# Kernel tuning notes

Hardware: AMD Instinct MI355X
Metric: run time of the kernel (lower is better)

Reference implementation:

```python
import jax, jax.numpy as jnp
import numpy as np

B, T, D, U = 16, 4096, 256, 256
ZR = 0.1  # zoneout_rate; inference: h_t = h_cand + ZR*(h_prev - h_cand)


def setup_inputs() -> dict:
    key = jax.random.key(0)
    ks = jax.random.split(key, 16)
    def rn(k, shape, s):
        return (jax.random.normal(k, shape, jnp.float32) * s).astype(jnp.float32)
    inp = {"x": jax.random.normal(ks[0], (B, T, D), jnp.float32)}
    dims = [D, U, U]
    i = 1
    for l in range(3):
        inp[f"W{l}"] = rn(ks[i], (dims[l], 3 * U), 0.05); i += 1
        inp[f"U{l}"] = rn(ks[i], (U, 3 * U), 0.05); i += 1
        inp[f"b{l}"] = rn(ks[i], (2, 3 * U), 0.02); i += 1
        inp[f"h0_{l}"] = rn(ks[i], (1, U), 1.0); i += 1  # learnable_state: N(0,1)
    inp["Wd"] = rn(ks[i], (U, D), 0.05); i += 1
    inp["bd"] = rn(ks[i], (D,), 0.02)
    return inp


def _gru_zoneout_layer(x, W, Uk, b, h0):
    """x: [B,T,in]; Keras GRU reset_after=True, gate order (z,r,h).
    Returns sequence of h_cand (cell outputs); carried state is zoneouted."""
    b_in, b_rec = b[0], b[1]
    xg = jnp.einsum('bti,ig->btg', x, W) + b_in  # [B,T,3U] precomputed input gates
    h_init = jnp.broadcast_to(h0, (x.shape[0], h0.shape[-1]))

    def step(h, xg_t):
        rg = h @ Uk + b_rec                       # [B,3U]
        xz, xr, xh = jnp.split(xg_t, 3, axis=-1)
        rz, rr, rh = jnp.split(rg, 3, axis=-1)
        z = jax.nn.sigmoid(xz + rz)
        r = jax.nn.sigmoid(xr + rr)
        hh = jnp.tanh(xh + r * rh)
        h_cand = z * h + (1.0 - z) * hh           # cell output
        h_new = h_cand + ZR * (h - h_cand)        # zoneout (inference)
        return h_new, h_cand

    _, ys = jax.lax.scan(step, h_init, jnp.swapaxes(xg, 0, 1))  # [T,B,U]
    return jnp.swapaxes(ys, 0, 1)


def reference(x, W0, U0, b0, h0_0, W1, U1, b1, h0_1, W2, U2, b2, h0_2, Wd, bd):
    y = _gru_zoneout_layer(x, W0, U0, b0, h0_0)
    y = y + _gru_zoneout_layer(y, W1, U1, b1, h0_1)   # residual, factor 1.0
    y = y + _gru_zoneout_layer(y, W2, U2, b2, h0_2)
    return jnp.einsum('btu,ud->btd', y, Wd) + bd      # linear dense head
```

## Files before the change

kernel.cpp:

```cpp
#include <hip/hip_runtime.h>
#include <cstdint>
#include <cstddef>

#define ZONEOUT 0.1f

typedef __attribute__((ext_vector_type(8))) short bf16x8;
typedef __attribute__((ext_vector_type(4))) float f32x4;
typedef __attribute__((ext_vector_type(4))) unsigned short u16x4;
typedef __attribute__((ext_vector_type(8))) unsigned short u16x8;
typedef __attribute__((ext_vector_type(4))) float float4_;

static constexpr int BB = 16;
static constexpr int TT = 4096;
static constexpr int DD = 256;
static constexpr int UU = 256;
static constexpr int GG = 768;
static constexpr int STR = 280;

__device__ __forceinline__ unsigned short f2bf(float f) {
  unsigned int u = __builtin_bit_cast(unsigned int, f);
  u = u + 0x7fffu + ((u >> 16) & 1u);
  return (unsigned short)(u >> 16);
}
__device__ __forceinline__ float bf2f(unsigned short s) {
  unsigned int u = ((unsigned int)s) << 16;
  return __builtin_bit_cast(float, u);
}
__device__ __forceinline__ float sigm(float x) {
  float e = __builtin_amdgcn_exp2f(-1.4426950408889634f * x);
  return __builtin_amdgcn_rcpf(1.0f + e);
}
__device__ __forceinline__ float tanh_(float x) {
  float e = __builtin_amdgcn_exp2f(2.8853900817779268f * x);
  return 1.0f - 2.0f * __builtin_amdgcn_rcpf(1.0f + e);
}

__device__ __forceinline__ void wg_barrier_lds() {
  asm volatile("s_waitcnt lgkmcnt(0)\n\ts_barrier" ::: "memory");
}

__global__ void transpose_cast_kernel(const float* __restrict__ src,
                                      unsigned short* __restrict__ dst,
                                      int K, int N) {
  int idx = blockIdx.x * blockDim.x + threadIdx.x;
  int total = K * N;
  if (idx < total) {
    int k = idx / N, n = idx - k * N;
    dst[(size_t)n * K + k] = f2bf(src[idx]);
  }
}

__launch_bounds__(256, 2)
__global__ void gates_gemm_kernel(const float* __restrict__ In,
                                  const unsigned short* __restrict__ Wt,
                                  const float* __restrict__ bin,
                                  unsigned short* __restrict__ xgp) {
  __shared__ unsigned short Asm[64 * STR];
  __shared__ unsigned short Bsm[64 * STR];
  const int m0 = blockIdx.x * 64;
  const int n0 = blockIdx.y * 64;
  const int tid = threadIdx.x;
  {
    int row = tid >> 2, cb = (tid & 3) * 64;
    const float* src = In + (size_t)(m0 + row) * DD + cb;
#pragma unroll
    for (int i = 0; i < 16; ++i) {
      float4_ v = *(const float4_*)(src + i * 4);
      u16x4 o;
      o.x = f2bf(v.x); o.y = f2bf(v.y); o.z = f2bf(v.z); o.w = f2bf(v.w);
      *(u16x4*)(&Asm[row * STR + cb + i * 4]) = o;
    }
  }
  {
#pragma unroll
    for (int i = 0; i < 8; ++i) {
      int c = i * 256 + tid;
      int row = c >> 5, part = c & 31;
      u16x8 v = *(const u16x8*)(Wt + (size_t)(n0 + row) * 256 + part * 8);
      *(u16x8*)(&Bsm[row * STR + part * 8]) = v;
    }
  }
  __syncthreads();
  const int w = tid >> 6, l = tid & 63, lr = l & 15, lg = l >> 4;
  f32x4 acc[4] = {};
#pragma unroll
  for (int k0 = 0; k0 < 8; ++k0) {
    bf16x8 a = *(const bf16x8*)(&Asm[(16 * w + lr) * STR + 32 * k0 + 8 * lg]);
#pragma unroll
    for (int ti = 0; ti < 4; ++ti) {
      bf16x8 b = *(const bf16x8*)(&Bsm[(16 * ti + lr) * STR + 32 * k0 + 8 * lg]);
      acc[ti] = __builtin_amdgcn_mfma_f32_16x16x32_bf16(a, b, acc[ti], 0, 0, 0);
    }
  }
#pragma unroll
  for (int ti = 0; ti < 4; ++ti) {
    int gcol = n0 + 16 * ti + lr;
    float bias = bin[gcol];
    int u = gcol & 255, slot = gcol >> 8;
#pragma unroll
    for (int r = 0; r < 4; ++r) {
      int m = m0 + 16 * w + 4 * lg + r;
      xgp[(size_t)m * 1024 + u * 4 + slot] = f2bf(acc[ti][r] + bias);
    }
  }
}

__launch_bounds__(256, 2)
__global__ void head_gemm_kernel(float* __restrict__ y,
                                 const unsigned short* __restrict__ Wdt,
                                 const float* __restrict__ bd) {
  __shared__ unsigned short Asm[64 * STR];
  const int m0 = blockIdx.x * 64;
  const int tid = threadIdx.x;
  {
    int row = tid >> 2, cb = (tid & 3) * 64;
    const float* src = y + (size_t)(m0 + row) * UU + cb;
#pragma unroll
    for (int i = 0; i < 16; ++i) {
      float4_ v = *(const float4_*)(src + i * 4);
      u16x4 o;
      o.x = f2bf(v.x); o.y = f2bf(v.y); o.z = f2bf(v.z); o.w = f2bf(v.w);
      *(u16x4*)(&Asm[row * STR + cb + i * 4]) = o;
    }
  }
  __syncthreads();
  const int w = tid >> 6, l = tid & 63, lr = l & 15, lg = l >> 4;
  f32x4 acc[16] = {};
#pragma unroll
  for (int k0 = 0; k0 < 8; ++k0) {
    bf16x8 a = *(const bf16x8*)(&Asm[(16 * w + lr) * STR + 32 * k0 + 8 * lg]);
#pragma unroll
    for (int ti = 0; ti < 16; ++ti) {
      bf16x8 b = *(const bf16x8*)(Wdt + (size_t)(16 * ti + lr) * 256 + 32 * k0 + 8 * lg);
      acc[ti] = __builtin_amdgcn_mfma_f32_16x16x32_bf16(a, b, acc[ti], 0, 0, 0);
    }
  }
#pragma unroll
  for (int ti = 0; ti < 16; ++ti) {
    int n = 16 * ti + lr;
    float bias = bd[n];
#pragma unroll
    for (int r = 0; r < 4; ++r) {
      int m = m0 + 16 * w + 4 * lg + r;
      y[(size_t)m * DD + n] = acc[ti][r] + bias;
    }
  }
}

__global__ void __attribute__((amdgpu_flat_work_group_size(512, 512), amdgpu_num_vgpr(256)))
gru_scan_kernel(const unsigned short* __restrict__ xgp,
                const unsigned short* __restrict__ Ut,
                const float* __restrict__ brec,
                const float* __restrict__ h0,
                float* __restrict__ y,
                int resid) {
  __shared__ unsigned short Utail[GG * 72];
  __shared__ unsigned short Hsm[2][BB * STR];

  const int tid = threadIdx.x;
  const int w = tid >> 6;
  const int l = tid & 63;
  const int lr = l & 15;
  const int lg = l >> 4;

  for (int i = 0; i < 12; ++i) {
    int c = i * 512 + tid;
    int row = c >> 3, part = c & 7;
    u16x8 v = *(const u16x8*)(Ut + (size_t)row * 256 + 192 + part * 8);
    *(u16x8*)(&Utail[row * 72 + part * 8]) = v;
  }

  f32x4 ufr[2][3][6];
  float bias[2][3];
#pragma unroll
  for (int tri = 0; tri < 2; ++tri) {
    int u = 32 * w + 16 * tri + lr;
#pragma unroll
    for (int g = 0; g < 3; ++g) {
      int n = g * 256 + u;
      bias[tri][g] = brec[n];
#pragma unroll
      for (int k0 = 0; k0 < 6; ++k0)
        ufr[tri][g][k0] = *(const f32x4*)(Ut + (size_t)n * 256 + 32 * k0 + 8 * lg);
    }
  }
#pragma unroll
  for (int tri = 0; tri < 2; ++tri)
#pragma unroll
    for (int g = 0; g < 3; ++g)
#pragma unroll
      for (int k0 = 0; k0 < 6; ++k0)
        asm volatile("" : "+v"(ufr[tri][g][k0]));

  float hprev[2][4];
#pragma unroll
  for (int tri = 0; tri < 2; ++tri) {
    int u = 32 * w + 16 * tri + lr;
    float hv = h0[u];
#pragma unroll
    for (int r = 0; r < 4; ++r) {
      hprev[tri][r] = hv;
      int b = 4 * lg + r;
      Hsm[0][b * STR + u] = f2bf(hv);
    }
  }

  u16x4 xv[2][4];
#pragma unroll
  for (int tri = 0; tri < 2; ++tri) {
    int u = 32 * w + 16 * tri + lr;
#pragma unroll
    for (int r = 0; r < 4; ++r) {
      int b = 4 * lg + r;
      xv[tri][r] = *(const u16x4*)(xgp + ((size_t)b * TT) * 1024 + u * 4);
    }
  }
  wg_barrier_lds();

  for (int t = 0; t < TT; ++t) {
    const unsigned short* cur = &Hsm[t & 1][0];
    unsigned short* nxt = &Hsm[(t + 1) & 1][0];

    float ypref[2][4];
    if (resid) {
#pragma unroll
      for (int tri = 0; tri < 2; ++tri) {
        int u = 32 * w + 16 * tri + lr;
#pragma unroll
        for (int r = 0; r < 4; ++r) {
          int b = 4 * lg + r;
          ypref[tri][r] = y[((size_t)b * TT + t) * UU + u];
        }
      }
    }

    f32x4 acc[2][3];
#pragma unroll
    for (int tri = 0; tri < 2; ++tri)
#pragma unroll
      for (int g = 0; g < 3; ++g) {
        float bv = bias[tri][g];
        acc[tri][g] = (f32x4){bv, bv, bv, bv};
      }
#pragma unroll
    for (int k0 = 0; k0 < 8; ++k0) {
      bf16x8 a = *(const bf16x8*)(&cur[lr * STR + 32 * k0 + 8 * lg]);
      if (k0 < 6) {
#pragma unroll
        for (int tri = 0; tri < 2; ++tri)
#pragma unroll
          for (int g = 0; g < 3; ++g)
            acc[tri][g] = __builtin_amdgcn_mfma_f32_16x16x32_bf16(
                a, __builtin_bit_cast(bf16x8, ufr[tri][g][k0]), acc[tri][g], 0, 0, 0);
      } else {
#pragma unroll
        for (int tri = 0; tri < 2; ++tri)
#pragma unroll
          for (int g = 0; g < 3; ++g) {
            int n = g * 256 + 32 * w + 16 * tri + lr;
            bf16x8 bfr = *(const bf16x8*)(&Utail[n * 72 + (k0 - 6) * 32 + 8 * lg]);
            acc[tri][g] = __builtin_amdgcn_mfma_f32_16x16x32_bf16(a, bfr, acc[tri][g], 0, 0, 0);
          }
      }
    }

    const int tn = (t + 1 < TT) ? t + 1 : t;
#pragma unroll
    for (int tri = 0; tri < 2; ++tri) {
      int u = 32 * w + 16 * tri + lr;
#pragma unroll
      for (int r = 0; r < 4; ++r) {
        int b = 4 * lg + r;
        u16x4 xvv = xv[tri][r];
        xv[tri][r] = *(const u16x4*)(xgp + ((size_t)b * TT + tn) * 1024 + u * 4);
        float xz = bf2f(xvv.x), xr = bf2f(xvv.y), xh = bf2f(xvv.z);
        float h = hprev[tri][r];
        float z = sigm(xz + acc[tri][0][r]);
        float rg = sigm(xr + acc[tri][1][r]);
        float hh = tanh_(xh + rg * acc[tri][2][r]);
        float cand = hh + z * (h - hh);
        float hnew = cand + ZONEOUT * (h - cand);
        hprev[tri][r] = hnew;
        nxt[b * STR + u] = f2bf(hnew);
        float ov = cand;
        if (resid) ov += ypref[tri][r];
        y[((size_t)b * TT + t) * UU + u] = ov;
      }
    }
    wg_barrier_lds();
  }
}

extern "C" void kernel_launch(void* const* d_in, const int* in_sizes, int n_in,
                              void* d_out, int out_size, void* d_ws, size_t ws_size,
                              hipStream_t stream) {
  const float* x = (const float*)d_in[0];
  const float* W[3]  = {(const float*)d_in[1], (const float*)d_in[5], (const float*)d_in[9]};
  const float* Um[3] = {(const float*)d_in[2], (const float*)d_in[6], (const float*)d_in[10]};
  const float* bm[3] = {(const float*)d_in[3], (const float*)d_in[7], (const float*)d_in[11]};
  const float* h0m[3] = {(const float*)d_in[4], (const float*)d_in[8], (const float*)d_in[12]};
  const float* Wd = (const float*)d_in[13];
  const float* bd = (const float*)d_in[14];
  float* out = (float*)d_out;

  char* ws = (char*)d_ws;
  unsigned short* xgp = (unsigned short*)ws;
  size_t off = (size_t)65536 * 1024 * 2;
  unsigned short* Ut[3];
  unsigned short* Wt[3];
  for (int l = 0; l < 3; ++l) { Ut[l] = (unsigned short*)(ws + off); off += (size_t)768 * 256 * 2; }
  for (int l = 0; l < 3; ++l) { Wt[l] = (unsigned short*)(ws + off); off += (size_t)768 * 256 * 2; }
  unsigned short* Wdt = (unsigned short*)(ws + off); off += (size_t)256 * 256 * 2;

  const int tgrid = (768 * 256 + 255) / 256;
  for (int l = 0; l < 3; ++l) {
    hipLaunchKernelGGL(transpose_cast_kernel, dim3(tgrid), dim3(256), 0, stream, Um[l], Ut[l], 256, 768);
    hipLaunchKernelGGL(transpose_cast_kernel, dim3(tgrid), dim3(256), 0, stream, W[l], Wt[l], 256, 768);
  }
  hipLaunchKernelGGL(transpose_cast_kernel, dim3((256 * 256 + 255) / 256), dim3(256), 0, stream,
                     Wd, Wdt, 256, 256);

  for (int l = 0; l < 3; ++l) {
    const float* in_l = (l == 0) ? x : out;
    hipLaunchKernelGGL(gates_gemm_kernel, dim3(1024, 12), dim3(256), 0, stream,
                       in_l, Wt[l], bm[l], xgp);
    hipLaunchKernelGGL(gru_scan_kernel, dim3(1), dim3(512), 0, stream,
                       xgp, Ut[l], bm[l] + 768, h0m[l], out, l ? 1 : 0);
  }
  hipLaunchKernelGGL(head_gemm_kernel, dim3(1024), dim3(256), 0, stream, out, Wdt, bd);
}
```

Measured before the change: 28.20 ms.

## Split GRU scan across 16 waves with one 16-unit tile each

The single-workgroup recurrent scan grows from 8 waves of 512 threads to 16 waves of 1024 threads. Each wave now owns one 16-unit column tile instead of two, which halves per-wave MFMA work and register-resident U fragments on the serial critical path. LDS strides for the hidden state and the U tail also change (280 to 282, 72 to 70) to alter the bank mapping. The cost is a barrier across twice as many waves every timestep and a lower per-thread register budget, since the explicit 256-VGPR attribute is dropped.

```diff
diff --git a/kernel.cpp b/kernel.cpp
--- a/kernel.cpp
+++ b/kernel.cpp
@@ -15,7 +15,8 @@
 static constexpr int DD = 256;
 static constexpr int UU = 256;
 static constexpr int GG = 768;
-static constexpr int STR = 280;
+static constexpr int STR = 282;
+static constexpr int UTS = 70;
 
 __device__ __forceinline__ unsigned short f2bf(float f) {
   unsigned int u = __builtin_bit_cast(unsigned int, f);
@@ -147,14 +148,14 @@
   }
 }
 
-__global__ void __attribute__((amdgpu_flat_work_group_size(512, 512), amdgpu_num_vgpr(256)))
+__global__ void __attribute__((amdgpu_flat_work_group_size(1024, 1024)))
 gru_scan_kernel(const unsigned short* __restrict__ xgp,
                 const unsigned short* __restrict__ Ut,
                 const float* __restrict__ brec,
                 const float* __restrict__ h0,
                 float* __restrict__ y,
                 int resid) {
-  __shared__ unsigned short Utail[GG * 72];
+  __shared__ unsigned short Utail[GG * UTS];
   __shared__ unsigned short Hsm[2][BB * STR];
 
   const int tid = threadIdx.x;
@@ -162,58 +163,48 @@
   const int l = tid & 63;
   const int lr = l & 15;
   const int lg = l >> 4;
-
-  for (int i = 0; i < 12; ++i) {
-    int c = i * 512 + tid;
+  const int u = 16 * w + lr;
+
+#pragma unroll
+  for (int i = 0; i < 6; ++i) {
+    int c = i * 1024 + tid;
     int row = c >> 3, part = c & 7;
     u16x8 v = *(const u16x8*)(Ut + (size_t)row * 256 + 192 + part * 8);
-    *(u16x8*)(&Utail[row * 72 + part * 8]) = v;
-  }
-
-  f32x4 ufr[2][3][6];
-  float bias[2][3];
-#pragma unroll
-  for (int tri = 0; tri < 2; ++tri) {
-    int u = 32 * w + 16 * tri + lr;
-#pragma unroll
-    for (int g = 0; g < 3; ++g) {
-      int n = g * 256 + u;
-      bias[tri][g] = brec[n];
-#pragma unroll
-      for (int k0 = 0; k0 < 6; ++k0)
-        ufr[tri][g][k0] = *(const f32x4*)(Ut + (size_t)n * 256 + 32 * k0 + 8 * lg);
-    }
-  }
-#pragma unroll
-  for (int tri = 0; tri < 2; ++tri)
-#pragma unroll
-    for (int g = 0; g < 3; ++g)
-#pragma unroll
-      for (int k0 = 0; k0 < 6; ++k0)
-        asm volatile("" : "+v"(ufr[tri][g][k0]));
-
-  float hprev[2][4];
-#pragma unroll
-  for (int tri = 0; tri < 2; ++tri) {
-    int u = 32 * w + 16 * tri + lr;
+    *(u16x8*)(&Utail[row * UTS + part * 8]) = v;
+  }
+
+  f32x4 ufr[3][6];
+  float bias[3];
+#pragma unroll
+  for (int g = 0; g < 3; ++g) {
+    int n = g * 256 + u;
+    bias[g] = brec[n];
+#pragma unroll
+    for (int k0 = 0; k0 < 6; ++k0)
+      ufr[g][k0] = *(const f32x4*)(Ut + (size_t)n * 256 + 32 * k0 + 8 * lg);
+  }
+#pragma unroll
+  for (int g = 0; g < 3; ++g)
+#pragma unroll
+    for (int k0 = 0; k0 < 6; ++k0)
+      asm volatile("" : "+v"(ufr[g][k0]));
+
+  float hprev[4];
+  {
     float hv = h0[u];
 #pragma unroll
     for (int r = 0; r < 4; ++r) {
-      hprev[tri][r] = hv;
+      hprev[r] = hv;
       int b = 4 * lg + r;
       Hsm[0][b * STR + u] = f2bf(hv);
     }
   }
 
-  u16x4 xv[2][4];
-#pragma unroll
-  for (int tri = 0; tri < 2; ++tri) {
-    int u = 32 * w + 16 * tri + lr;
-#pragma unroll
-    for (int r = 0; r < 4; ++r) {
-      int b = 4 * lg + r;
-      xv[tri][r] = *(const u16x4*)(xgp + ((size_t)b * TT) * 1024 + u * 4);
-    }
+  u16x4 xv[4];
+#pragma unroll
+  for (int r = 0; r < 4; ++r) {
+    int b = 4 * lg + r;
+    xv[r] = *(const u16x4*)(xgp + ((size_t)b * TT) * 1024 + u * 4);
   }
   wg_barrier_lds();
 
@@ -221,71 +212,57 @@
     const unsigned short* cur = &Hsm[t & 1][0];
     unsigned short* nxt = &Hsm[(t + 1) & 1][0];
 
-    float ypref[2][4];
+    float ypref[4];
     if (resid) {
 #pragma unroll
-      for (int tri = 0; tri < 2; ++tri) {
-        int u = 32 * w + 16 * tri + lr;
-#pragma unroll
-        for (int r = 0; r < 4; ++r) {
-          int b = 4 * lg + r;
-          ypref[tri][r] = y[((size_t)b * TT + t) * UU + u];
-        }
+      for (int r = 0; r < 4; ++r) {
+        int b = 4 * lg + r;
+        ypref[r] = y[((size_t)b * TT + t) * UU + u];
       }
     }
 
-    f32x4 acc[2][3];
-#pragma unroll
-    for (int tri = 0; tri < 2; ++tri)
-#pragma unroll
-      for (int g = 0; g < 3; ++g) {
-        float bv = bias[tri][g];
-        acc[tri][g] = (f32x4){bv, bv, bv, bv};
-      }
+    f32x4 acc[3];
+#pragma unroll
+    for (int g = 0; g < 3; ++g) {
+      float bv = bias[g];
+      acc[g] = (f32x4){bv, bv, bv, bv};
+    }
 #pragma unroll
     for (int k0 = 0; k0 < 8; ++k0) {
       bf16x8 a = *(const bf16x8*)(&cur[lr * STR + 32 * k0 + 8 * lg]);
       if (k0 < 6) {
 #pragma unroll
-        for (int tri = 0; tri < 2; ++tri)
-#pragma unroll
-          for (int g = 0; g < 3; ++g)
-            acc[tri][g] = __builtin_amdgcn_mfma_f32_16x16x32_bf16(
-                a, __builtin_bit_cast(bf16x8, ufr[tri][g][k0]), acc[tri][g], 0, 0, 0);
+        for (int g = 0; g < 3; ++g)
+          acc[g] = __builtin_amdgcn_mfma_f32_16x16x32_bf16(
+              a, __builtin_bit_cast(bf16x8, ufr[g][k0]), acc[g], 0, 0, 0);
       } else {
 #pragma unroll
-        for (int tri = 0; tri < 2; ++tri)
-#pragma unroll
-          for (int g = 0; g < 3; ++g) {
-            int n = g * 256 + 32 * w + 16 * tri + lr;
-            bf16x8 bfr = *(const bf16x8*)(&Utail[n * 72 + (k0 - 6) * 32 + 8 * lg]);
-            acc[tri][g] = __builtin_amdgcn_mfma_f32_16x16x32_bf16(a, bfr, acc[tri][g], 0, 0, 0);
-          }
+        for (int g = 0; g < 3; ++g) {
+          int n = g * 256 + u;
+          bf16x8 bfr = *(const bf16x8*)(&Utail[n * UTS + (k0 - 6) * 32 + 8 * lg]);
+          acc[g] = __builtin_amdgcn_mfma_f32_16x16x32_bf16(a, bfr, acc[g], 0, 0, 0);
+        }
       }
     }
 
     const int tn = (t + 1 < TT) ? t + 1 : t;
 #pragma unroll
-    for (int tri = 0; tri < 2; ++tri) {
-      int u = 32 * w + 16 * tri + lr;
-#pragma unroll
-      for (int r = 0; r < 4; ++r) {
-        int b = 4 * lg + r;
-        u16x4 xvv = xv[tri][r];
-        xv[tri][r] = *(const u16x4*)(xgp + ((size_t)b * TT + tn) * 1024 + u * 4);
-        float xz = bf2f(xvv.x), xr = bf2f(xvv.y), xh = bf2f(xvv.z);
-        float h = hprev[tri][r];
-        float z = sigm(xz + acc[tri][0][r]);
-        float rg = sigm(xr + acc[tri][1][r]);
-        float hh = tanh_(xh + rg * acc[tri][2][r]);
-        float cand = hh + z * (h - hh);
-        float hnew = cand + ZONEOUT * (h - cand);
-        hprev[tri][r] = hnew;
-        nxt[b * STR + u] = f2bf(hnew);
-        float ov = cand;
-        if (resid) ov += ypref[tri][r];
-        y[((size_t)b * TT + t) * UU + u] = ov;
-      }
+    for (int r = 0; r < 4; ++r) {
+      int b = 4 * lg + r;
+      u16x4 xvv = xv[r];
+      xv[r] = *(const u16x4*)(xgp + ((size_t)b * TT + tn) * 1024 + u * 4);
+      float xz = bf2f(xvv.x), xr = bf2f(xvv.y), xh = bf2f(xvv.z);
+      float h = hprev[r];
+      float z = sigm(xz + acc[0][r]);
+      float rg = sigm(xr + acc[1][r]);
+      float hh = tanh_(xh + rg * acc[2][r]);
+      float cand = hh + z * (h - hh);
+      float hnew = cand + ZONEOUT * (h - cand);
+      hprev[r] = hnew;
+      nxt[b * STR + u] = f2bf(hnew);
+      float ov = cand;
+      if (resid) ov += ypref[r];
+      y[((size_t)b * TT + t) * UU + u] = ov;
     }
     wg_barrier_lds();
   }
@@ -324,7 +301,7 @@
     const float* in_l = (l == 0) ? x : out;
     hipLaunchKernelGGL(gates_gemm_kernel, dim3(1024, 12), dim3(256), 0, stream,
                        in_l, Wt[l], bm[l], xgp);
-    hipLaunchKernelGGL(gru_scan_kernel, dim3(1), dim3(512), 0, stream,
+    hipLaunchKernelGGL(gru_scan_kernel, dim3(1), dim3(1024), 0, stream,
                        xgp, Ut[l], bm[l] + 768, h0m[l], out, l ? 1 : 0);
   }
   hipLaunchKernelGGL(head_gemm_kernel, dim3(1024), dim3(256), 0, stream, out, Wdt, bd);
```

Result: slower. 62.08 ms (+120.2%).

## Keep full recurrent weights in AGPRs, fold z/r recurrent bias into input gates

Applied to the files above, without the earlier changes.

The scan kernel now holds all 8 k-slices of the recurrent weight fragments in registers, with an accumulator-register ('a') constraint in place of VGPRs. This removes the LDS Utail copy and the per-step LDS loads for the last two k-chunks. The z and r recurrent biases are folded into the precomputed input-gate GEMM, so the accumulators start at zero and only the h-gate bias is added after the matmul. The LDS row stride also changes from 280 to 282. The larger register footprint risks spills, or extra AGPR-to-VGPR moves if MFMA B operands cannot be read straight from AGPRs, and the odd stride may misalign the 16-byte LDS vector loads.

```diff
diff --git a/kernel.cpp b/kernel.cpp
--- a/kernel.cpp
+++ b/kernel.cpp
@@ -15,7 +15,7 @@
 static constexpr int DD = 256;
 static constexpr int UU = 256;
 static constexpr int GG = 768;
-static constexpr int STR = 280;
+static constexpr int STR = 282;
 
 __device__ __forceinline__ unsigned short f2bf(float f) {
   unsigned int u = __builtin_bit_cast(unsigned int, f);
@@ -54,6 +54,7 @@
 __global__ void gates_gemm_kernel(const float* __restrict__ In,
                                   const unsigned short* __restrict__ Wt,
                                   const float* __restrict__ bin,
+                                  const float* __restrict__ brec,
                                   unsigned short* __restrict__ xgp) {
   __shared__ unsigned short Asm[64 * STR];
   __shared__ unsigned short Bsm[64 * STR];
@@ -95,8 +96,8 @@
 #pragma unroll
   for (int ti = 0; ti < 4; ++ti) {
     int gcol = n0 + 16 * ti + lr;
-    float bias = bin[gcol];
     int u = gcol & 255, slot = gcol >> 8;
+    float bias = bin[gcol] + (slot < 2 ? brec[gcol] : 0.0f);
 #pragma unroll
     for (int r = 0; r < 4; ++r) {
       int m = m0 + 16 * w + 4 * lg + r;
@@ -147,14 +148,13 @@
   }
 }
 
-__global__ void __attribute__((amdgpu_flat_work_group_size(512, 512), amdgpu_num_vgpr(256)))
+__global__ void __attribute__((amdgpu_flat_work_group_size(512, 512)))
 gru_scan_kernel(const unsigned short* __restrict__ xgp,
                 const unsigned short* __restrict__ Ut,
                 const float* __restrict__ brec,
                 const float* __restrict__ h0,
                 float* __restrict__ y,
                 int resid) {
-  __shared__ unsigned short Utail[GG * 72];
   __shared__ unsigned short Hsm[2][BB * STR];
 
   const int tid = threadIdx.x;
@@ -163,24 +163,17 @@
   const int lr = l & 15;
   const int lg = l >> 4;
 
-  for (int i = 0; i < 12; ++i) {
-    int c = i * 512 + tid;
-    int row = c >> 3, part = c & 7;
-    u16x8 v = *(const u16x8*)(Ut + (size_t)row * 256 + 192 + part * 8);
-    *(u16x8*)(&Utail[row * 72 + part * 8]) = v;
-  }
-
-  f32x4 ufr[2][3][6];
-  float bias[2][3];
+  f32x4 ufr[2][3][8];
+  float bias_h[2];
 #pragma unroll
   for (int tri = 0; tri < 2; ++tri) {
     int u = 32 * w + 16 * tri + lr;
+    bias_h[tri] = brec[512 + u];
 #pragma unroll
     for (int g = 0; g < 3; ++g) {
       int n = g * 256 + u;
-      bias[tri][g] = brec[n];
-#pragma unroll
-      for (int k0 = 0; k0 < 6; ++k0)
+#pragma unroll
+      for (int k0 = 0; k0 < 8; ++k0)
         ufr[tri][g][k0] = *(const f32x4*)(Ut + (size_t)n * 256 + 32 * k0 + 8 * lg);
     }
   }
@@ -189,8 +182,8 @@
 #pragma unroll
     for (int g = 0; g < 3; ++g)
 #pragma unroll
-      for (int k0 = 0; k0 < 6; ++k0)
-        asm volatile("" : "+v"(ufr[tri][g][k0]));
+      for (int k0 = 0; k0 < 8; ++k0)
+        asm volatile("" : "+a"(ufr[tri][g][k0]));
 
   float hprev[2][4];
 #pragma unroll
@@ -234,34 +227,16 @@
       }
     }
 
-    f32x4 acc[2][3];
-#pragma unroll
-    for (int tri = 0; tri < 2; ++tri)
-#pragma unroll
-      for (int g = 0; g < 3; ++g) {
-        float bv = bias[tri][g];
-        acc[tri][g] = (f32x4){bv, bv, bv, bv};
-      }
+    f32x4 acc[2][3] = {};
 #pragma unroll
     for (int k0 = 0; k0 < 8; ++k0) {
       bf16x8 a = *(const bf16x8*)(&cur[lr * STR + 32 * k0 + 8 * lg]);
-      if (k0 < 6) {
-#pragma unroll
-        for (int tri = 0; tri < 2; ++tri)
-#pragma unroll
-          for (int g = 0; g < 3; ++g)
-            acc[tri][g] = __builtin_amdgcn_mfma_f32_16x16x32_bf16(
-                a, __builtin_bit_cast(bf16x8, ufr[tri][g][k0]), acc[tri][g], 0, 0, 0);
-      } else {
-#pragma unroll
-        for (int tri = 0; tri < 2; ++tri)
-#pragma unroll
-          for (int g = 0; g < 3; ++g) {
-            int n = g * 256 + 32 * w + 16 * tri + lr;
-            bf16x8 bfr = *(const bf16x8*)(&Utail[n * 72 + (k0 - 6) * 32 + 8 * lg]);
-            acc[tri][g] = __builtin_amdgcn_mfma_f32_16x16x32_bf16(a, bfr, acc[tri][g], 0, 0, 0);
-          }
-      }
+#pragma unroll
+      for (int tri = 0; tri < 2; ++tri)
+#pragma unroll
+        for (int g = 0; g < 3; ++g)
+          acc[tri][g] = __builtin_amdgcn_mfma_f32_16x16x32_bf16(
+              a, __builtin_bit_cast(bf16x8, ufr[tri][g][k0]), acc[tri][g], 0, 0, 0);
     }
 
     const int tn = (t + 1 < TT) ? t + 1 : t;
@@ -277,7 +252,7 @@
         float h = hprev[tri][r];
         float z = sigm(xz + acc[tri][0][r]);
         float rg = sigm(xr + acc[tri][1][r]);
-        float hh = tanh_(xh + rg * acc[tri][2][r]);
+        float hh = tanh_(xh + rg * (acc[tri][2][r] + bias_h[tri]));
         float cand = hh + z * (h - hh);
         float hnew = cand + ZONEOUT * (h - cand);
         hprev[tri][r] = hnew;
@@ -323,7 +298,7 @@
   for (int l = 0; l < 3; ++l) {
     const float* in_l = (l == 0) ? x : out;
     hipLaunchKernelGGL(gates_gemm_kernel, dim3(1024, 12), dim3(256), 0, stream,
-                       in_l, Wt[l], bm[l], xgp);
+                       in_l, Wt[l], bm[l], bm[l] + 768, xgp);
     hipLaunchKernelGGL(gru_scan_kernel, dim3(1), dim3(512), 0, stream,
                        xgp, Ut[l], bm[l] + 768, h0m[l], out, l ? 1 : 0);
   }
```

New measurement: 56.96 ms. 2.02x slower.
